# Optimization experiments

Hardware: AMD Instinct MI355X
Metric: run time of the kernel (lower is better)

Reference implementation:

```python
import jax, jax.numpy as jnp
import numpy as np

CLIP = 7.0          # cfg.swiglu_clip
AUX_COEF = 0.02     # cfg.router_aux_loss_coef
TOP_K = 4           # cfg.experts_per_token


def setup_inputs() -> dict:
    key = jax.random.key(0)
    ks = jax.random.split(key, 4)
    H, E, FF = 1024, 16, 1024
    B, T = 2, 1024
    std = 0.02
    return {
        "x": jax.random.normal(ks[0], (B, T, H), jnp.float32),
        "W_in": jax.random.normal(ks[1], (E, H, 2 * FF), jnp.float32) * std,
        "b_in": jnp.zeros((E, 2 * FF), jnp.float32),
        "W_out": jax.random.normal(ks[2], (E, FF, H), jnp.float32) * std,
        "b_out": jnp.zeros((E, H), jnp.float32),
        "router_w": jax.random.normal(ks[3], (E, H), jnp.float32) * std,
        "router_b": jnp.zeros((E,), jnp.float32),
    }


def reference(x, W_in, b_in, W_out, b_out, router_w, router_b):
    B, T, H = x.shape
    E = W_in.shape[0]
    S = B * T
    x_flat = x.reshape(S, H)

    # --- router + top-k gating ---
    logits = x_flat @ router_w.T + router_b                         # [S, E]
    topk_w, topk_i = jax.lax.top_k(logits, TOP_K)                   # [S, K]
    topk_w = jax.nn.softmax(topk_w.astype(jnp.float32), axis=-1).astype(x.dtype)

    # --- aux load-balance loss (faithful to source, incl. argmax-over-indices) ---
    probs = jax.nn.softmax(logits.astype(jnp.float32), axis=-1)     # [S, E]
    importance = probs.mean(axis=0)                                 # [E]
    load = jax.nn.one_hot(jnp.argmax(topk_i, axis=-1), E, dtype=jnp.float32).mean(axis=0)
    aux_loss = AUX_COEF * E * jnp.sum(importance * load)

    # scatter top-k weights to dense [S, E] combine weights
    final_w = jnp.zeros((S, E), x.dtype).at[jnp.arange(S)[:, None], topk_i].add(topk_w)

    # --- dense per-expert SwiGLU FFN (every expert for every token) ---
    h = jnp.einsum('sh,ehd->sed', x_flat, W_in) + b_in              # [S, E, 2*FF]
    up, gate = jnp.split(h, 2, axis=-1)                             # chunk(2, -1)
    up = jnp.clip(up, -CLIP, CLIP)
    gate = jnp.clip(gate, -CLIP, CLIP)
    act = jax.nn.silu(gate) * up                                    # [S, E, FF]
    eo = jnp.einsum('sef,efh->seh', act, W_out) + b_out             # [S, E, H]

    out = jnp.einsum('seh,se->sh', eo, final_w).reshape(B, T, H)
    return out, aux_loss
```

## Files before the change

### kernel.cpp

```cpp
#include <hip/hip_runtime.h>
#include <math.h>

#define S_TOK 2048
#define H_DIM 1024
#define E_NUM 16
#define FF_DIM 1024
#define TOPK 4
#define CLIPV 7.0f
#define AUXC 0.02f
#define BK 32
#define NT (H_DIM / BK)

typedef short bf16x8 __attribute__((ext_vector_type(8)));
typedef float f32x4 __attribute__((ext_vector_type(4)));

__device__ __forceinline__ unsigned short f2bf(float f) {
  unsigned int u = __float_as_uint(f);
  u += 0x7fffu + ((u >> 16) & 1u);
  return (unsigned short)(u >> 16);
}

__device__ __forceinline__ void gload16(const void* g, void* l) {
  __builtin_amdgcn_global_load_lds((const __attribute__((address_space(1))) void*)g,
                                   (__attribute__((address_space(3))) void*)l, 16, 0, 0);
}

__device__ __forceinline__ int imin(int a, int b) { return a < b ? a : b; }

__global__ void logits_kernel(const float* __restrict__ x, const float* __restrict__ rw,
                              const float* __restrict__ rb, float* __restrict__ logits,
                              unsigned short* __restrict__ xb) {
  int tok = blockIdx.x * 4 + (threadIdx.x >> 6);
  int lane = threadIdx.x & 63;
  const float4* xr = (const float4*)(x + (size_t)tok * H_DIM);
  ushort4* xbw = (ushort4*)(xb + (size_t)tok * H_DIM);
  float p[E_NUM];
#pragma unroll
  for (int e = 0; e < E_NUM; ++e) p[e] = 0.f;
#pragma unroll
  for (int it = 0; it < 4; ++it) {
    float4 xv = xr[it * 64 + lane];
    ushort4 o;
    o.x = f2bf(xv.x); o.y = f2bf(xv.y); o.z = f2bf(xv.z); o.w = f2bf(xv.w);
    xbw[it * 64 + lane] = o;
#pragma unroll
    for (int e = 0; e < E_NUM; ++e) {
      float4 wv = ((const float4*)(rw + (size_t)e * H_DIM))[it * 64 + lane];
      p[e] += xv.x * wv.x + xv.y * wv.y + xv.z * wv.z + xv.w * wv.w;
    }
  }
#pragma unroll
  for (int e = 0; e < E_NUM; ++e) {
#pragma unroll
    for (int off = 32; off > 0; off >>= 1) p[e] += __shfl_xor(p[e], off);
  }
  if (lane == 0) {
    float4* lp = (float4*)&logits[tok * E_NUM];
#pragma unroll
    for (int q = 0; q < 4; ++q)
      lp[q] = make_float4(p[q * 4 + 0] + rb[q * 4 + 0], p[q * 4 + 1] + rb[q * 4 + 1],
                          p[q * 4 + 2] + rb[q * 4 + 2], p[q * 4 + 3] + rb[q * 4 + 3]);
  }
}

__global__ __launch_bounds__(256) void topk_kernel(const float* __restrict__ logits,
                                                   int* __restrict__ topk_i, float* __restrict__ topk_w,
                                                   int* __restrict__ counts, float* __restrict__ imp,
                                                   int* __restrict__ pos_cnt) {
  __shared__ float s_imp[E_NUM];
  __shared__ int s_cnt[E_NUM];
  __shared__ int s_pos[TOPK];
  int tid = threadIdx.x;
  if (tid < E_NUM) { s_imp[tid] = 0.f; s_cnt[tid] = 0; }
  if (tid < TOPK) s_pos[tid] = 0;
  __syncthreads();

  int t = blockIdx.x * 256 + tid;
  float lg[E_NUM];
  {
    const float4* lp = (const float4*)&logits[t * E_NUM];
#pragma unroll
    for (int q = 0; q < 4; ++q) {
      float4 v = lp[q];
      lg[q * 4 + 0] = v.x; lg[q * 4 + 1] = v.y; lg[q * 4 + 2] = v.z; lg[q * 4 + 3] = v.w;
    }
  }
  int idx[TOPK]; float val[TOPK];
  float tmp[E_NUM];
#pragma unroll
  for (int e = 0; e < E_NUM; ++e) tmp[e] = lg[e];
#pragma unroll
  for (int k = 0; k < TOPK; ++k) {
    float best = -INFINITY; int bi = 0;
#pragma unroll
    for (int e = 0; e < E_NUM; ++e) if (tmp[e] > best) { best = tmp[e]; bi = e; }
    val[k] = best; idx[k] = bi; tmp[bi] = -INFINITY;
  }
  float ssum = 0.f, wv[TOPK];
#pragma unroll
  for (int k = 0; k < TOPK; ++k) { wv[k] = expf(val[k] - val[0]); ssum += wv[k]; }
#pragma unroll
  for (int k = 0; k < TOPK; ++k) wv[k] /= ssum;
#pragma unroll
  for (int k = 0; k < TOPK; ++k) {
    topk_i[t * TOPK + k] = idx[k];
    topk_w[t * TOPK + k] = wv[k];
  }
  float se = 0.f, pr[E_NUM];
#pragma unroll
  for (int e = 0; e < E_NUM; ++e) { pr[e] = expf(lg[e] - val[0]); se += pr[e]; }
  float inv = 1.f / se;
  int mi = idx[0], pos = 0;
#pragma unroll
  for (int k = 1; k < TOPK; ++k) if (idx[k] > mi) { mi = idx[k]; pos = k; }

  int lane = tid & 63;
#pragma unroll
  for (int e = 0; e < E_NUM; ++e) {
    float v = pr[e] * inv;
    int c = (idx[0] == e) + (idx[1] == e) + (idx[2] == e) + (idx[3] == e);
#pragma unroll
    for (int off = 32; off > 0; off >>= 1) {
      v += __shfl_xor(v, off);
      c += __shfl_xor(c, off);
    }
    if (lane == 0) {
      atomicAdd(&s_imp[e], v);
      atomicAdd(&s_cnt[e], c);
    }
  }
#pragma unroll
  for (int k = 0; k < TOPK; ++k) {
    int pc = (pos == k) ? 1 : 0;
#pragma unroll
    for (int off = 32; off > 0; off >>= 1) pc += __shfl_xor(pc, off);
    if (lane == 0) atomicAdd(&s_pos[k], pc);
  }
  __syncthreads();
  if (tid < E_NUM) {
    atomicAdd(&imp[tid], s_imp[tid]);
    atomicAdd(&counts[tid], s_cnt[tid]);
  }
  if (tid < TOPK) atomicAdd(&pos_cnt[tid], s_pos[tid]);
}

__global__ void scan_kernel(const int* __restrict__ counts, int* __restrict__ offsets) {
  if (threadIdx.x == 0) {
    int off = 0;
    for (int e = 0; e < E_NUM; ++e) { offsets[e] = off; off += counts[e]; }
    offsets[E_NUM] = off;
  }
}

__global__ __launch_bounds__(256) void assign_kernel(
    const int* __restrict__ topk_i, const float* __restrict__ topk_w,
    const int* __restrict__ offsets, int* __restrict__ cursor,
    int* __restrict__ tok_list, float* __restrict__ w_list) {
  __shared__ int s_cnt[E_NUM];
  __shared__ int s_base[E_NUM];
  int tid = threadIdx.x;
  if (tid < E_NUM) s_cnt[tid] = 0;
  __syncthreads();
  int t = blockIdx.x * 256 + tid;
  int e[TOPK], lslot[TOPK];
#pragma unroll
  for (int k = 0; k < TOPK; ++k) {
    e[k] = topk_i[t * TOPK + k];
    lslot[k] = atomicAdd(&s_cnt[e[k]], 1);
  }
  __syncthreads();
  if (tid < E_NUM) s_base[tid] = atomicAdd(&cursor[tid], s_cnt[tid]);
  __syncthreads();
#pragma unroll
  for (int k = 0; k < TOPK; ++k) {
    int slot = offsets[e[k]] + s_base[e[k]] + lslot[k];
    tok_list[slot] = t;
    w_list[slot] = topk_w[t * TOPK + k];
  }
}

__global__ void transpose_kernel(const float* __restrict__ in, unsigned short* __restrict__ out,
                                 int R, int C) {
  __shared__ float tile[64][65];
  int e = blockIdx.z;
  in  += (size_t)e * R * C;
  out += (size_t)e * R * C;
  int r0 = blockIdx.y * 64, c0 = blockIdx.x * 64;
  int tx = threadIdx.x & 15, ty = threadIdx.x >> 4;
#pragma unroll
  for (int j = 0; j < 4; ++j) {
    int r = ty + j * 16;
    float4 v = *(const float4*)&in[(size_t)(r0 + r) * C + c0 + tx * 4];
    tile[r][tx * 4 + 0] = v.x; tile[r][tx * 4 + 1] = v.y;
    tile[r][tx * 4 + 2] = v.z; tile[r][tx * 4 + 3] = v.w;
  }
  __syncthreads();
#pragma unroll
  for (int j = 0; j < 4; ++j) {
    int c = ty + j * 16;
    ushort4 o;
    o.x = f2bf(tile[tx * 4 + 0][c]);
    o.y = f2bf(tile[tx * 4 + 1][c]);
    o.z = f2bf(tile[tx * 4 + 2][c]);
    o.w = f2bf(tile[tx * 4 + 3][c]);
    *(ushort4*)&out[(size_t)(c0 + c) * R + r0 + tx * 4] = o;
  }
}

__global__ __launch_bounds__(256) void gemm1_kernel(
    const unsigned short* __restrict__ xb, const unsigned short* __restrict__ winT,
    const float* __restrict__ b_in, const int* __restrict__ offsets,
    const int* __restrict__ tok_list, unsigned short* __restrict__ act) {
  __shared__ unsigned short ldsA[2][128 * BK];
  __shared__ unsigned short ldsB[2][128 * BK];
  const int e = blockIdx.z;
  const int base = offsets[e];
  const int cnt = offsets[e + 1] - base;
  const int mt = blockIdx.y;
  if (mt * 128 >= cnt) return;
  const int n0 = blockIdx.x * 64;
  const int tid = threadIdx.x, w = tid >> 6, lane = tid & 63;

  const int srow0 = w * 32 + (lane >> 2);
  const int srow1 = srow0 + 16;
  const int t0 = tok_list[base + imin(mt * 128 + srow0, cnt - 1)];
  const int t1 = tok_list[base + imin(mt * 128 + srow1, cnt - 1)];
  const unsigned short* gA0 = xb + (size_t)t0 * H_DIM + (lane & 3) * 8;
  const unsigned short* gA1 = xb + (size_t)t1 * H_DIM + (lane & 3) * 8;
  auto nbmap = [&](int c) {
    int f = n0 + (c >> 5) * 16 + (c & 15);
    return ((c >> 4) & 1) ? (FF_DIM + f) : f;
  };
  const unsigned short* we = winT + (size_t)e * 2 * FF_DIM * H_DIM;
  const unsigned short* gB0 = we + (size_t)nbmap(srow0) * H_DIM + (lane & 3) * 8;
  const unsigned short* gB1 = we + (size_t)nbmap(srow1) * H_DIM + (lane & 3) * 8;

  f32x4 acc[4][4];
#pragma unroll
  for (int m = 0; m < 4; ++m)
#pragma unroll
    for (int n = 0; n < 4; ++n) acc[m][n] = (f32x4){0.f, 0.f, 0.f, 0.f};

#define STAGE1(buf, k0)                                        \
  do {                                                         \
    gload16(gA0 + (k0), &ldsA[buf][(w * 32 + 0) * BK]);        \
    gload16(gA1 + (k0), &ldsA[buf][(w * 32 + 16) * BK]);       \
    gload16(gB0 + (k0), &ldsB[buf][(w * 32 + 0) * BK]);        \
    gload16(gB1 + (k0), &ldsB[buf][(w * 32 + 16) * BK]);       \
  } while (0)

  STAGE1(0, 0);
  __syncthreads();
  int buf = 0;
  const int ko = (lane >> 4) * 8;
  const int wm = (w >> 1) * 64, wn = (w & 1) * 64;
  for (int kt = 0; kt < NT; ++kt) {
    if (kt + 1 < NT) STAGE1(buf ^ 1, (kt + 1) * BK);
    bf16x8 a[4], b[4];
#pragma unroll
    for (int mf = 0; mf < 4; ++mf)
      a[mf] = *(const bf16x8*)&ldsA[buf][(wm + mf * 16 + (lane & 15)) * BK + ko];
#pragma unroll
    for (int nf = 0; nf < 4; ++nf)
      b[nf] = *(const bf16x8*)&ldsB[buf][(wn + nf * 16 + (lane & 15)) * BK + ko];
#pragma unroll
    for (int mf = 0; mf < 4; ++mf)
#pragma unroll
      for (int nf = 0; nf < 4; ++nf)
        acc[mf][nf] = __builtin_amdgcn_mfma_f32_16x16x32_bf16(a[mf], b[nf], acc[mf][nf], 0, 0, 0);
    __syncthreads();
    buf ^= 1;
  }

  const float* bin = b_in + (size_t)e * 2 * FF_DIM;
#pragma unroll
  for (int mf = 0; mf < 4; ++mf) {
    int rbase = wm + mf * 16 + (lane >> 4) * 4;
#pragma unroll
    for (int p = 0; p < 2; ++p) {
      int f = n0 + (wn >> 1) + p * 16 + (lane & 15);
      float bu = bin[f], bg = bin[FF_DIM + f];
#pragma unroll
      for (int i = 0; i < 4; ++i) {
        int mrow = mt * 128 + rbase + i;
        if (mrow < cnt) {
          float up = acc[mf][2 * p][i] + bu;
          float gt = acc[mf][2 * p + 1][i] + bg;
          up = fminf(fmaxf(up, -CLIPV), CLIPV);
          gt = fminf(fmaxf(gt, -CLIPV), CLIPV);
          float av = (gt / (1.f + expf(-gt))) * up;
          act[(size_t)(base + mrow) * FF_DIM + f] = f2bf(av);
        }
      }
    }
  }
}

__global__ __launch_bounds__(256) void gemm2_kernel(
    const unsigned short* __restrict__ act, const unsigned short* __restrict__ woutT,
    const float* __restrict__ b_out, const int* __restrict__ offsets,
    const int* __restrict__ tok_list, const float* __restrict__ w_list,
    float* __restrict__ out) {
  __shared__ unsigned short ldsA[2][128 * BK];
  __shared__ unsigned short ldsB[2][128 * BK];
  const int e = blockIdx.z;
  const int base = offsets[e];
  const int cnt = offsets[e + 1] - base;
  const int mt = blockIdx.y;
  if (mt * 128 >= cnt) return;
  const int n0 = blockIdx.x * 128;
  const int tid = threadIdx.x, w = tid >> 6, lane = tid & 63;

  const int srow0 = w * 32 + (lane >> 2);
  const int srow1 = srow0 + 16;
  const int m0_ = imin(mt * 128 + srow0, cnt - 1);
  const int m1_ = imin(mt * 128 + srow1, cnt - 1);
  const unsigned short* gA0 = act + (size_t)(base + m0_) * FF_DIM + (lane & 3) * 8;
  const unsigned short* gA1 = act + (size_t)(base + m1_) * FF_DIM + (lane & 3) * 8;
  const unsigned short* we = woutT + (size_t)e * H_DIM * FF_DIM;
  const unsigned short* gB0 = we + (size_t)(n0 + srow0) * FF_DIM + (lane & 3) * 8;
  const unsigned short* gB1 = we + (size_t)(n0 + srow1) * FF_DIM + (lane & 3) * 8;

  f32x4 acc[4][4];
#pragma unroll
  for (int m = 0; m < 4; ++m)
#pragma unroll
    for (int n = 0; n < 4; ++n) acc[m][n] = (f32x4){0.f, 0.f, 0.f, 0.f};

#define STAGE2(buf, k0)                                        \
  do {                                                         \
    gload16(gA0 + (k0), &ldsA[buf][(w * 32 + 0) * BK]);        \
    gload16(gA1 + (k0), &ldsA[buf][(w * 32 + 16) * BK]);       \
    gload16(gB0 + (k0), &ldsB[buf][(w * 32 + 0) * BK]);        \
    gload16(gB1 + (k0), &ldsB[buf][(w * 32 + 16) * BK]);       \
  } while (0)

  STAGE2(0, 0);
  __syncthreads();
  int buf = 0;
  const int ko = (lane >> 4) * 8;
  const int wm = (w >> 1) * 64, wn = (w & 1) * 64;
  for (int kt = 0; kt < FF_DIM / BK; ++kt) {
    if (kt + 1 < FF_DIM / BK) STAGE2(buf ^ 1, (kt + 1) * BK);
    bf16x8 a[4], b[4];
#pragma unroll
    for (int mf = 0; mf < 4; ++mf)
      a[mf] = *(const bf16x8*)&ldsA[buf][(wm + mf * 16 + (lane & 15)) * BK + ko];
#pragma unroll
    for (int nf = 0; nf < 4; ++nf)
      b[nf] = *(const bf16x8*)&ldsB[buf][(wn + nf * 16 + (lane & 15)) * BK + ko];
#pragma unroll
    for (int mf = 0; mf < 4; ++mf)
#pragma unroll
      for (int nf = 0; nf < 4; ++nf)
        acc[mf][nf] = __builtin_amdgcn_mfma_f32_16x16x32_bf16(a[mf], b[nf], acc[mf][nf], 0, 0, 0);
    __syncthreads();
    buf ^= 1;
  }

  const float* bo = b_out + (size_t)e * H_DIM;
#pragma unroll
  for (int mf = 0; mf < 4; ++mf) {
#pragma unroll
    for (int i = 0; i < 4; ++i) {
      int mrow = mt * 128 + wm + mf * 16 + (lane >> 4) * 4 + i;
      if (mrow < cnt) {
        int slot = base + mrow;
        int t = tok_list[slot];
        float wt = w_list[slot];
#pragma unroll
        for (int nf = 0; nf < 4; ++nf) {
          int h = n0 + wn + nf * 16 + (lane & 15);
          atomicAdd(&out[(size_t)t * H_DIM + h], wt * (acc[mf][nf][i] + bo[h]));
        }
      }
    }
  }
}

__global__ void finalize_kernel(const float* __restrict__ imp, const int* __restrict__ pos_cnt,
                                float* __restrict__ out_aux) {
  if (threadIdx.x == 0) {
    float s = 0.f;
    for (int p = 0; p < TOPK; ++p)
      s += (imp[p] / (float)S_TOK) * ((float)pos_cnt[p] / (float)S_TOK);
    *out_aux = AUXC * (float)E_NUM * s;
  }
}

extern "C" void kernel_launch(void* const* d_in, const int* in_sizes, int n_in,
                              void* d_out, int out_size, void* d_ws, size_t ws_size,
                              hipStream_t stream) {
  const float* x     = (const float*)d_in[0];
  const float* W_in  = (const float*)d_in[1];
  const float* b_in  = (const float*)d_in[2];
  const float* W_out = (const float*)d_in[3];
  const float* b_out = (const float*)d_in[4];
  const float* rw    = (const float*)d_in[5];
  const float* rb    = (const float*)d_in[6];
  float* out = (float*)d_out;

  char* ws = (char*)d_ws;
  size_t off = 0;
  auto alloc = [&](size_t bytes) {
    void* p = ws + off;
    off = (off + bytes + 255) & ~(size_t)255;
    return p;
  };
  unsigned short* xb    = (unsigned short*)alloc((size_t)S_TOK * H_DIM * 2);
  unsigned short* winT  = (unsigned short*)alloc((size_t)E_NUM * 2 * FF_DIM * H_DIM * 2);
  unsigned short* woutT = (unsigned short*)alloc((size_t)E_NUM * H_DIM * FF_DIM * 2);
  unsigned short* act   = (unsigned short*)alloc((size_t)S_TOK * TOPK * FF_DIM * 2);
  float* logits  = (float*)alloc((size_t)S_TOK * E_NUM * 4);
  int*   topk_i  = (int*)alloc(S_TOK * TOPK * 4);
  float* topk_w  = (float*)alloc(S_TOK * TOPK * 4);
  int*   tok_list= (int*)alloc(S_TOK * TOPK * 4);
  float* w_list  = (float*)alloc(S_TOK * TOPK * 4);
  int* ctrl = (int*)alloc(64 * 4);
  int* counts = ctrl;
  int* cursor = ctrl + 16;
  int* pos_cnt = ctrl + 32;
  float* imp = (float*)(ctrl + 48);
  int* offsets = (int*)alloc(32 * 4);

  hipMemsetAsync(d_out, 0, (size_t)out_size * sizeof(float), stream);
  hipMemsetAsync(ctrl, 0, 64 * 4, stream);

  logits_kernel<<<S_TOK / 4, 256, 0, stream>>>(x, rw, rb, logits, xb);
  transpose_kernel<<<dim3(2 * FF_DIM / 64, H_DIM / 64, E_NUM), 256, 0, stream>>>(W_in, winT, H_DIM, 2 * FF_DIM);
  transpose_kernel<<<dim3(H_DIM / 64, FF_DIM / 64, E_NUM), 256, 0, stream>>>(W_out, woutT, FF_DIM, H_DIM);
  topk_kernel<<<S_TOK / 256, 256, 0, stream>>>(logits, topk_i, topk_w, counts, imp, pos_cnt);
  scan_kernel<<<1, 64, 0, stream>>>(counts, offsets);
  assign_kernel<<<S_TOK / 256, 256, 0, stream>>>(topk_i, topk_w, offsets, cursor, tok_list, w_list);
  gemm1_kernel<<<dim3(FF_DIM / 64, S_TOK / 128, E_NUM), 256, 0, stream>>>(xb, winT, b_in, offsets, tok_list, act);
  gemm2_kernel<<<dim3(H_DIM / 128, S_TOK / 128, E_NUM), 256, 0, stream>>>(act, woutT, b_out, offsets, tok_list, w_list, out);
  finalize_kernel<<<1, 64, 0, stream>>>(imp, pos_cnt, out + (size_t)S_TOK * H_DIM);
}
```

Measured before the change: 228.7 us.

## Enlarge grouped GEMM tiles to 128x256, add split-K and XCD-aware block remap

Both expert GEMMs move from 128x128 to 128x256 output tiles, with each wave computing an 8x4 grid of MFMA fragments. The aim is more reuse of the A and B tiles held in LDS. gemm2 splits K into two halves that both atomically add into the output, with bias added only by the first half, so it keeps enough blocks in flight. Both grids are flattened to 1D and remapped so that consecutive block IDs spread across the XCDs. The costs are more accumulator registers (launch bounds set to 2 blocks), more LDS per block, and twice as many atomics in gemm2.

```diff
diff --git a/kernel.cpp b/kernel.cpp
--- a/kernel.cpp
+++ b/kernel.cpp
@@ -207,64 +207,69 @@
   }
 }
 
-__global__ __launch_bounds__(256) void gemm1_kernel(
+__global__ __launch_bounds__(256, 2) void gemm1_kernel(
     const unsigned short* __restrict__ xb, const unsigned short* __restrict__ winT,
     const float* __restrict__ b_in, const int* __restrict__ offsets,
     const int* __restrict__ tok_list, unsigned short* __restrict__ act) {
   __shared__ unsigned short ldsA[2][128 * BK];
-  __shared__ unsigned short ldsB[2][128 * BK];
-  const int e = blockIdx.z;
+  __shared__ unsigned short ldsB[2][256 * BK];
+  const int lin = blockIdx.x;
+  const int nid = (lin & 7) * 256 + (lin >> 3);
+  const int e  = nid >> 7;
+  const int mt = (nid & 127) >> 3;
+  const int nt = nid & 7;
   const int base = offsets[e];
   const int cnt = offsets[e + 1] - base;
-  const int mt = blockIdx.y;
   if (mt * 128 >= cnt) return;
-  const int n0 = blockIdx.x * 64;
+  const int n0f = nt * 128;
   const int tid = threadIdx.x, w = tid >> 6, lane = tid & 63;
 
-  const int srow0 = w * 32 + (lane >> 2);
-  const int srow1 = srow0 + 16;
-  const int t0 = tok_list[base + imin(mt * 128 + srow0, cnt - 1)];
-  const int t1 = tok_list[base + imin(mt * 128 + srow1, cnt - 1)];
+  const int arow = w * 16 + (lane >> 2);
+  const int t0 = tok_list[base + imin(mt * 128 + arow, cnt - 1)];
+  const int t1 = tok_list[base + imin(mt * 128 + arow + 64, cnt - 1)];
   const unsigned short* gA0 = xb + (size_t)t0 * H_DIM + (lane & 3) * 8;
   const unsigned short* gA1 = xb + (size_t)t1 * H_DIM + (lane & 3) * 8;
-  auto nbmap = [&](int c) {
-    int f = n0 + (c >> 5) * 16 + (c & 15);
-    return ((c >> 4) & 1) ? (FF_DIM + f) : f;
+  auto brow_f = [&](int r) {
+    int f = n0f + ((r >> 5) << 4) + (r & 15);
+    return ((r >> 4) & 1) ? (FF_DIM + f) : f;
   };
   const unsigned short* we = winT + (size_t)e * 2 * FF_DIM * H_DIM;
-  const unsigned short* gB0 = we + (size_t)nbmap(srow0) * H_DIM + (lane & 3) * 8;
-  const unsigned short* gB1 = we + (size_t)nbmap(srow1) * H_DIM + (lane & 3) * 8;
-
-  f32x4 acc[4][4];
-#pragma unroll
-  for (int m = 0; m < 4; ++m)
+  const unsigned short* gB0 = we + (size_t)brow_f(arow)       * H_DIM + (lane & 3) * 8;
+  const unsigned short* gB1 = we + (size_t)brow_f(arow + 64)  * H_DIM + (lane & 3) * 8;
+  const unsigned short* gB2 = we + (size_t)brow_f(arow + 128) * H_DIM + (lane & 3) * 8;
+  const unsigned short* gB3 = we + (size_t)brow_f(arow + 192) * H_DIM + (lane & 3) * 8;
+
+  f32x4 acc[8][4];
+#pragma unroll
+  for (int m = 0; m < 8; ++m)
 #pragma unroll
     for (int n = 0; n < 4; ++n) acc[m][n] = (f32x4){0.f, 0.f, 0.f, 0.f};
 
-#define STAGE1(buf, k0)                                        \
-  do {                                                         \
-    gload16(gA0 + (k0), &ldsA[buf][(w * 32 + 0) * BK]);        \
-    gload16(gA1 + (k0), &ldsA[buf][(w * 32 + 16) * BK]);       \
-    gload16(gB0 + (k0), &ldsB[buf][(w * 32 + 0) * BK]);        \
-    gload16(gB1 + (k0), &ldsB[buf][(w * 32 + 16) * BK]);       \
+#define STAGE1(buf, k0)                                     \
+  do {                                                      \
+    gload16(gA0 + (k0), &ldsA[buf][w * 512]);               \
+    gload16(gA1 + (k0), &ldsA[buf][w * 512 + 2048]);        \
+    gload16(gB0 + (k0), &ldsB[buf][w * 512]);               \
+    gload16(gB1 + (k0), &ldsB[buf][w * 512 + 2048]);        \
+    gload16(gB2 + (k0), &ldsB[buf][w * 512 + 4096]);        \
+    gload16(gB3 + (k0), &ldsB[buf][w * 512 + 6144]);        \
   } while (0)
 
   STAGE1(0, 0);
   __syncthreads();
   int buf = 0;
   const int ko = (lane >> 4) * 8;
-  const int wm = (w >> 1) * 64, wn = (w & 1) * 64;
   for (int kt = 0; kt < NT; ++kt) {
     if (kt + 1 < NT) STAGE1(buf ^ 1, (kt + 1) * BK);
-    bf16x8 a[4], b[4];
-#pragma unroll
-    for (int mf = 0; mf < 4; ++mf)
-      a[mf] = *(const bf16x8*)&ldsA[buf][(wm + mf * 16 + (lane & 15)) * BK + ko];
+    bf16x8 a[8], b[4];
+#pragma unroll
+    for (int mf = 0; mf < 8; ++mf)
+      a[mf] = *(const bf16x8*)&ldsA[buf][(mf * 16 + (lane & 15)) * BK + ko];
 #pragma unroll
     for (int nf = 0; nf < 4; ++nf)
-      b[nf] = *(const bf16x8*)&ldsB[buf][(wn + nf * 16 + (lane & 15)) * BK + ko];
-#pragma unroll
-    for (int mf = 0; mf < 4; ++mf)
+      b[nf] = *(const bf16x8*)&ldsB[buf][(w * 64 + nf * 16 + (lane & 15)) * BK + ko];
+#pragma unroll
+    for (int mf = 0; mf < 8; ++mf)
 #pragma unroll
       for (int nf = 0; nf < 4; ++nf)
         acc[mf][nf] = __builtin_amdgcn_mfma_f32_16x16x32_bf16(a[mf], b[nf], acc[mf][nf], 0, 0, 0);
@@ -274,11 +279,11 @@
 
   const float* bin = b_in + (size_t)e * 2 * FF_DIM;
 #pragma unroll
-  for (int mf = 0; mf < 4; ++mf) {
-    int rbase = wm + mf * 16 + (lane >> 4) * 4;
+  for (int mf = 0; mf < 8; ++mf) {
+    int rbase = mf * 16 + (lane >> 4) * 4;
 #pragma unroll
     for (int p = 0; p < 2; ++p) {
-      int f = n0 + (wn >> 1) + p * 16 + (lane & 15);
+      int f = n0f + (w * 2 + p) * 16 + (lane & 15);
       float bu = bin[f], bg = bin[FF_DIM + f];
 #pragma unroll
       for (int i = 0; i < 4; ++i) {
@@ -296,61 +301,69 @@
   }
 }
 
-__global__ __launch_bounds__(256) void gemm2_kernel(
+__global__ __launch_bounds__(256, 2) void gemm2_kernel(
     const unsigned short* __restrict__ act, const unsigned short* __restrict__ woutT,
     const float* __restrict__ b_out, const int* __restrict__ offsets,
     const int* __restrict__ tok_list, const float* __restrict__ w_list,
     float* __restrict__ out) {
   __shared__ unsigned short ldsA[2][128 * BK];
-  __shared__ unsigned short ldsB[2][128 * BK];
-  const int e = blockIdx.z;
+  __shared__ unsigned short ldsB[2][256 * BK];
+  const int lin = blockIdx.x;
+  const int nid = (lin & 7) * 256 + (lin >> 3);
+  const int e = nid >> 7;
+  const int rem = nid & 127;
+  const int mt = rem >> 3;
+  const int nt = (rem >> 1) & 3;
+  const int ks = rem & 1;
   const int base = offsets[e];
   const int cnt = offsets[e + 1] - base;
-  const int mt = blockIdx.y;
   if (mt * 128 >= cnt) return;
-  const int n0 = blockIdx.x * 128;
+  const int n0 = nt * 256;
   const int tid = threadIdx.x, w = tid >> 6, lane = tid & 63;
 
-  const int srow0 = w * 32 + (lane >> 2);
-  const int srow1 = srow0 + 16;
-  const int m0_ = imin(mt * 128 + srow0, cnt - 1);
-  const int m1_ = imin(mt * 128 + srow1, cnt - 1);
-  const unsigned short* gA0 = act + (size_t)(base + m0_) * FF_DIM + (lane & 3) * 8;
-  const unsigned short* gA1 = act + (size_t)(base + m1_) * FF_DIM + (lane & 3) * 8;
+  const int arow = w * 16 + (lane >> 2);
+  const int m0_ = imin(mt * 128 + arow, cnt - 1);
+  const int m1_ = imin(mt * 128 + arow + 64, cnt - 1);
+  const int kbase = ks * 512 + (lane & 3) * 8;
+  const unsigned short* gA0 = act + (size_t)(base + m0_) * FF_DIM + kbase;
+  const unsigned short* gA1 = act + (size_t)(base + m1_) * FF_DIM + kbase;
   const unsigned short* we = woutT + (size_t)e * H_DIM * FF_DIM;
-  const unsigned short* gB0 = we + (size_t)(n0 + srow0) * FF_DIM + (lane & 3) * 8;
-  const unsigned short* gB1 = we + (size_t)(n0 + srow1) * FF_DIM + (lane & 3) * 8;
-
-  f32x4 acc[4][4];
-#pragma unroll
-  for (int m = 0; m < 4; ++m)
+  const unsigned short* gB0 = we + (size_t)(n0 + arow)       * FF_DIM + kbase;
+  const unsigned short* gB1 = we + (size_t)(n0 + arow + 64)  * FF_DIM + kbase;
+  const unsigned short* gB2 = we + (size_t)(n0 + arow + 128) * FF_DIM + kbase;
+  const unsigned short* gB3 = we + (size_t)(n0 + arow + 192) * FF_DIM + kbase;
+
+  f32x4 acc[8][4];
+#pragma unroll
+  for (int m = 0; m < 8; ++m)
 #pragma unroll
     for (int n = 0; n < 4; ++n) acc[m][n] = (f32x4){0.f, 0.f, 0.f, 0.f};
 
-#define STAGE2(buf, k0)                                        \
-  do {                                                         \
-    gload16(gA0 + (k0), &ldsA[buf][(w * 32 + 0) * BK]);        \
-    gload16(gA1 + (k0), &ldsA[buf][(w * 32 + 16) * BK]);       \
-    gload16(gB0 + (k0), &ldsB[buf][(w * 32 + 0) * BK]);        \
-    gload16(gB1 + (k0), &ldsB[buf][(w * 32 + 16) * BK]);       \
+#define STAGE2(buf, k0)                                     \
+  do {                                                      \
+    gload16(gA0 + (k0), &ldsA[buf][w * 512]);               \
+    gload16(gA1 + (k0), &ldsA[buf][w * 512 + 2048]);        \
+    gload16(gB0 + (k0), &ldsB[buf][w * 512]);               \
+    gload16(gB1 + (k0), &ldsB[buf][w * 512 + 2048]);        \
+    gload16(gB2 + (k0), &ldsB[buf][w * 512 + 4096]);        \
+    gload16(gB3 + (k0), &ldsB[buf][w * 512 + 6144]);        \
   } while (0)
 
   STAGE2(0, 0);
   __syncthreads();
   int buf = 0;
   const int ko = (lane >> 4) * 8;
-  const int wm = (w >> 1) * 64, wn = (w & 1) * 64;
-  for (int kt = 0; kt < FF_DIM / BK; ++kt) {
-    if (kt + 1 < FF_DIM / BK) STAGE2(buf ^ 1, (kt + 1) * BK);
-    bf16x8 a[4], b[4];
-#pragma unroll
-    for (int mf = 0; mf < 4; ++mf)
-      a[mf] = *(const bf16x8*)&ldsA[buf][(wm + mf * 16 + (lane & 15)) * BK + ko];
+  for (int kt = 0; kt < 16; ++kt) {
+    if (kt + 1 < 16) STAGE2(buf ^ 1, (kt + 1) * BK);
+    bf16x8 a[8], b[4];
+#pragma unroll
+    for (int mf = 0; mf < 8; ++mf)
+      a[mf] = *(const bf16x8*)&ldsA[buf][(mf * 16 + (lane & 15)) * BK + ko];
 #pragma unroll
     for (int nf = 0; nf < 4; ++nf)
-      b[nf] = *(const bf16x8*)&ldsB[buf][(wn + nf * 16 + (lane & 15)) * BK + ko];
-#pragma unroll
-    for (int mf = 0; mf < 4; ++mf)
+      b[nf] = *(const bf16x8*)&ldsB[buf][(w * 64 + nf * 16 + (lane & 15)) * BK + ko];
+#pragma unroll
+    for (int mf = 0; mf < 8; ++mf)
 #pragma unroll
       for (int nf = 0; nf < 4; ++nf)
         acc[mf][nf] = __builtin_amdgcn_mfma_f32_16x16x32_bf16(a[mf], b[nf], acc[mf][nf], 0, 0, 0);
@@ -360,18 +373,19 @@
 
   const float* bo = b_out + (size_t)e * H_DIM;
 #pragma unroll
-  for (int mf = 0; mf < 4; ++mf) {
+  for (int mf = 0; mf < 8; ++mf) {
 #pragma unroll
     for (int i = 0; i < 4; ++i) {
-      int mrow = mt * 128 + wm + mf * 16 + (lane >> 4) * 4 + i;
+      int mrow = mt * 128 + mf * 16 + (lane >> 4) * 4 + i;
       if (mrow < cnt) {
         int slot = base + mrow;
         int t = tok_list[slot];
         float wt = w_list[slot];
 #pragma unroll
         for (int nf = 0; nf < 4; ++nf) {
-          int h = n0 + wn + nf * 16 + (lane & 15);
-          atomicAdd(&out[(size_t)t * H_DIM + h], wt * (acc[mf][nf][i] + bo[h]));
+          int h = n0 + w * 64 + nf * 16 + (lane & 15);
+          float v = acc[mf][nf][i] + (ks == 0 ? bo[h] : 0.f);
+          atomicAdd(&out[(size_t)t * H_DIM + h], wt * v);
         }
       }
     }
@@ -432,7 +446,7 @@
   topk_kernel<<<S_TOK / 256, 256, 0, stream>>>(logits, topk_i, topk_w, counts, imp, pos_cnt);
   scan_kernel<<<1, 64, 0, stream>>>(counts, offsets);
   assign_kernel<<<S_TOK / 256, 256, 0, stream>>>(topk_i, topk_w, offsets, cursor, tok_list, w_list);
-  gemm1_kernel<<<dim3(FF_DIM / 64, S_TOK / 128, E_NUM), 256, 0, stream>>>(xb, winT, b_in, offsets, tok_list, act);
-  gemm2_kernel<<<dim3(H_DIM / 128, S_TOK / 128, E_NUM), 256, 0, stream>>>(act, woutT, b_out, offsets, tok_list, w_list, out);
+  gemm1_kernel<<<2048, 256, 0, stream>>>(xb, winT, b_in, offsets, tok_list, act);
+  gemm2_kernel<<<2048, 256, 0, stream>>>(act, woutT, b_out, offsets, tok_list, w_list, out);
   finalize_kernel<<<1, 64, 0, stream>>>(imp, pos_cnt, out + (size_t)S_TOK * H_DIM);
 }
```

New measurement: 286.3 us. +25.2%, slower.

## Replace atomic scatter with per-slot expert output and gather combine kernel

Applied to the files above, without the earlier changes.

gemm2 now writes each routed row's expert output (plus bias) to a dense fp32 buffer instead of atomically adding weighted results into the output. A new combine kernel gathers each token's four slots via slot_of and sums them with the top-k weights, so the output memset is no longer needed. Both GEMM grids become 1D with a remapped block index that interleaves blocks across the work space, and launch bounds request 4 blocks per CU. This removes float atomics on the output but adds a 32 MB intermediate write and read.

```diff
diff --git a/kernel.cpp b/kernel.cpp
--- a/kernel.cpp
+++ b/kernel.cpp
@@ -153,9 +153,8 @@
 }
 
 __global__ __launch_bounds__(256) void assign_kernel(
-    const int* __restrict__ topk_i, const float* __restrict__ topk_w,
-    const int* __restrict__ offsets, int* __restrict__ cursor,
-    int* __restrict__ tok_list, float* __restrict__ w_list) {
+    const int* __restrict__ topk_i, const int* __restrict__ offsets, int* __restrict__ cursor,
+    int* __restrict__ tok_list, int* __restrict__ slot_of) {
   __shared__ int s_cnt[E_NUM];
   __shared__ int s_base[E_NUM];
   int tid = threadIdx.x;
@@ -175,7 +174,7 @@
   for (int k = 0; k < TOPK; ++k) {
     int slot = offsets[e[k]] + s_base[e[k]] + lslot[k];
     tok_list[slot] = t;
-    w_list[slot] = topk_w[t * TOPK + k];
+    slot_of[t * TOPK + k] = slot;
   }
 }
 
@@ -207,18 +206,21 @@
   }
 }
 
-__global__ __launch_bounds__(256) void gemm1_kernel(
+__global__ __launch_bounds__(256, 4) void gemm1_kernel(
     const unsigned short* __restrict__ xb, const unsigned short* __restrict__ winT,
     const float* __restrict__ b_in, const int* __restrict__ offsets,
     const int* __restrict__ tok_list, unsigned short* __restrict__ act) {
   __shared__ unsigned short ldsA[2][128 * BK];
   __shared__ unsigned short ldsB[2][128 * BK];
-  const int e = blockIdx.z;
+  const int lin = blockIdx.x;
+  const int nid = (lin & 7) * 512 + (lin >> 3);
+  const int e  = nid >> 8;
+  const int nt = (nid >> 4) & 15;
+  const int mt = nid & 15;
   const int base = offsets[e];
   const int cnt = offsets[e + 1] - base;
-  const int mt = blockIdx.y;
   if (mt * 128 >= cnt) return;
-  const int n0 = blockIdx.x * 64;
+  const int n0 = nt * 64;
   const int tid = threadIdx.x, w = tid >> 6, lane = tid & 63;
 
   const int srow0 = w * 32 + (lane >> 2);
@@ -296,19 +298,21 @@
   }
 }
 
-__global__ __launch_bounds__(256) void gemm2_kernel(
+__global__ __launch_bounds__(256, 4) void gemm2_kernel(
     const unsigned short* __restrict__ act, const unsigned short* __restrict__ woutT,
     const float* __restrict__ b_out, const int* __restrict__ offsets,
-    const int* __restrict__ tok_list, const float* __restrict__ w_list,
-    float* __restrict__ out) {
+    float* __restrict__ eo) {
   __shared__ unsigned short ldsA[2][128 * BK];
   __shared__ unsigned short ldsB[2][128 * BK];
-  const int e = blockIdx.z;
+  const int lin = blockIdx.x;
+  const int nid = (lin & 7) * 256 + (lin >> 3);
+  const int e = nid >> 7;
+  const int nt = (nid >> 4) & 7;
+  const int mt = nid & 15;
   const int base = offsets[e];
   const int cnt = offsets[e + 1] - base;
-  const int mt = blockIdx.y;
   if (mt * 128 >= cnt) return;
-  const int n0 = blockIdx.x * 128;
+  const int n0 = nt * 128;
   const int tid = threadIdx.x, w = tid >> 6, lane = tid & 63;
 
   const int srow0 = w * 32 + (lane >> 2);
@@ -365,17 +369,34 @@
     for (int i = 0; i < 4; ++i) {
       int mrow = mt * 128 + wm + mf * 16 + (lane >> 4) * 4 + i;
       if (mrow < cnt) {
-        int slot = base + mrow;
-        int t = tok_list[slot];
-        float wt = w_list[slot];
+        float* row = eo + (size_t)(base + mrow) * H_DIM;
 #pragma unroll
         for (int nf = 0; nf < 4; ++nf) {
           int h = n0 + wn + nf * 16 + (lane & 15);
-          atomicAdd(&out[(size_t)t * H_DIM + h], wt * (acc[mf][nf][i] + bo[h]));
+          row[h] = acc[mf][nf][i] + bo[h];
         }
       }
     }
   }
+}
+
+__global__ __launch_bounds__(256) void combine_kernel(
+    const float* __restrict__ eo, const float* __restrict__ topk_w,
+    const int* __restrict__ slot_of, float* __restrict__ out) {
+  int t = blockIdx.x;
+  int tid = threadIdx.x;
+  float4 r = make_float4(0.f, 0.f, 0.f, 0.f);
+#pragma unroll
+  for (int k = 0; k < TOPK; ++k) {
+    int s = slot_of[t * TOPK + k];
+    float wv = topk_w[t * TOPK + k];
+    float4 v = ((const float4*)(eo + (size_t)s * H_DIM))[tid];
+    r.x = fmaf(wv, v.x, r.x);
+    r.y = fmaf(wv, v.y, r.y);
+    r.z = fmaf(wv, v.z, r.z);
+    r.w = fmaf(wv, v.w, r.w);
+  }
+  ((float4*)(out + (size_t)t * H_DIM))[tid] = r;
 }
 
 __global__ void finalize_kernel(const float* __restrict__ imp, const int* __restrict__ pos_cnt,
@@ -411,11 +432,12 @@
   unsigned short* winT  = (unsigned short*)alloc((size_t)E_NUM * 2 * FF_DIM * H_DIM * 2);
   unsigned short* woutT = (unsigned short*)alloc((size_t)E_NUM * H_DIM * FF_DIM * 2);
   unsigned short* act   = (unsigned short*)alloc((size_t)S_TOK * TOPK * FF_DIM * 2);
+  float* eo      = (float*)alloc((size_t)S_TOK * TOPK * H_DIM * 4);
   float* logits  = (float*)alloc((size_t)S_TOK * E_NUM * 4);
   int*   topk_i  = (int*)alloc(S_TOK * TOPK * 4);
   float* topk_w  = (float*)alloc(S_TOK * TOPK * 4);
   int*   tok_list= (int*)alloc(S_TOK * TOPK * 4);
-  float* w_list  = (float*)alloc(S_TOK * TOPK * 4);
+  int*   slot_of = (int*)alloc(S_TOK * TOPK * 4);
   int* ctrl = (int*)alloc(64 * 4);
   int* counts = ctrl;
   int* cursor = ctrl + 16;
@@ -423,7 +445,6 @@
   float* imp = (float*)(ctrl + 48);
   int* offsets = (int*)alloc(32 * 4);
 
-  hipMemsetAsync(d_out, 0, (size_t)out_size * sizeof(float), stream);
   hipMemsetAsync(ctrl, 0, 64 * 4, stream);
 
   logits_kernel<<<S_TOK / 4, 256, 0, stream>>>(x, rw, rb, logits, xb);
@@ -431,8 +452,9 @@
   transpose_kernel<<<dim3(H_DIM / 64, FF_DIM / 64, E_NUM), 256, 0, stream>>>(W_out, woutT, FF_DIM, H_DIM);
   topk_kernel<<<S_TOK / 256, 256, 0, stream>>>(logits, topk_i, topk_w, counts, imp, pos_cnt);
   scan_kernel<<<1, 64, 0, stream>>>(counts, offsets);
-  assign_kernel<<<S_TOK / 256, 256, 0, stream>>>(topk_i, topk_w, offsets, cursor, tok_list, w_list);
-  gemm1_kernel<<<dim3(FF_DIM / 64, S_TOK / 128, E_NUM), 256, 0, stream>>>(xb, winT, b_in, offsets, tok_list, act);
-  gemm2_kernel<<<dim3(H_DIM / 128, S_TOK / 128, E_NUM), 256, 0, stream>>>(act, woutT, b_out, offsets, tok_list, w_list, out);
+  assign_kernel<<<S_TOK / 256, 256, 0, stream>>>(topk_i, offsets, cursor, tok_list, slot_of);
+  gemm1_kernel<<<4096, 256, 0, stream>>>(xb, winT, b_in, offsets, tok_list, act);
+  gemm2_kernel<<<2048, 256, 0, stream>>>(act, woutT, b_out, offsets, eo);
+  combine_kernel<<<S_TOK, 256, 0, stream>>>(eo, topk_w, slot_of, out);
   finalize_kernel<<<1, 64, 0, stream>>>(imp, pos_cnt, out + (size_t)S_TOK * H_DIM);
 }
```

Measured after the change: 199.3 us. 12.9% less time.
